# Kernel optimization log

Hardware: AMD Instinct MI355X
Metric: run time of the kernel (lower is better)

The kernel has to match this reference:

```python
import jax, jax.numpy as jnp
import numpy as np

M, N, D, H, R = 16384, 32, 128, 8, 237
Dh = D // H
SCALE = Dh ** -0.5
LN_EPS = 1e-5


def setup_inputs() -> dict:
    key = jax.random.key(0)
    ks = jax.random.split(key, 12)
    entity_repr = jax.random.normal(ks[0], (M, D), dtype=jnp.float32)
    neighbor_index = jax.random.randint(ks[1], (M, N), 0, M, dtype=jnp.int64)
    rel_ids = jax.random.randint(ks[2], (M, N), 0, R, dtype=jnp.int64)
    neighbor_mask = jax.random.randint(ks[3], (M, N), 0, 2, dtype=jnp.int32).astype(bool)
    neighbor_mask = neighbor_mask.at[:, 0].set(True)  # ensure >=1 valid neighbor per node
    s = 1.0 / np.sqrt(D)
    # weights stored in right-multiply form: y = x @ W + b
    Wq = jax.random.normal(ks[4], (D, D), dtype=jnp.float32) * s
    Wk = jax.random.normal(ks[5], (D, D), dtype=jnp.float32) * s
    Wv = jax.random.normal(ks[6], (D, D), dtype=jnp.float32) * s
    Wo = jax.random.normal(ks[7], (D, D), dtype=jnp.float32) * s
    bq = jnp.zeros((D,), jnp.float32)
    bk = jnp.zeros((D,), jnp.float32)
    bv = jnp.zeros((D,), jnp.float32)
    bo = jnp.zeros((D,), jnp.float32)
    rel_table = jax.random.normal(ks[8], (R, D), dtype=jnp.float32)
    ln_gamma = jnp.ones((D,), jnp.float32)
    ln_beta = jnp.zeros((D,), jnp.float32)
    return {
        "entity_repr": entity_repr, "neighbor_index": neighbor_index,
        "rel_ids": rel_ids, "neighbor_mask": neighbor_mask,
        "Wq": Wq, "bq": bq, "Wk": Wk, "bk": bk, "Wv": Wv, "bv": bv,
        "Wo": Wo, "bo": bo, "rel_table": rel_table,
        "ln_gamma": ln_gamma, "ln_beta": ln_beta,
    }


def _layernorm(x, gamma, beta):
    mu = jnp.mean(x, axis=-1, keepdims=True)
    var = jnp.var(x, axis=-1, keepdims=True)
    return (x - mu) * jax.lax.rsqrt(var + LN_EPS) * gamma + beta


def reference(entity_repr, neighbor_index, rel_ids, neighbor_mask,
              Wq, bq, Wk, bk, Wv, bv, Wo, bo, rel_table, ln_gamma, ln_beta):
    valid = neighbor_mask
    safe_index = jnp.where(valid, neighbor_index, 0)
    safe_rel = jnp.where(valid, rel_ids, 0)
    neighbor_repr = entity_repr[safe_index]          # [M, N, D] irregular gather
    rel_emb = rel_table[safe_rel]                     # [M, N, D]
    q = (entity_repr @ Wq + bq).reshape(M, H, Dh)     # [M, H, Dh] (query len 1)
    k = ((neighbor_repr + rel_emb) @ Wk + bk).reshape(M, N, H, Dh)
    v = (neighbor_repr @ Wv + bv).reshape(M, N, H, Dh)
    attn = jnp.einsum("mhd,mnhd->mhn", q, k) * SCALE  # [M, H, N]
    attn = jnp.where(valid[:, None, :], attn, -jnp.inf)
    attn = jax.nn.softmax(attn, axis=-1)
    attn = jnp.nan_to_num(attn, nan=0.0)
    out = jnp.einsum("mhn,mnhd->mhd", attn, v).reshape(M, D)
    out = out @ Wo + bo
    return _layernorm(entity_repr + out, ln_gamma, ln_beta)
```

## Files before the change

kernel.cpp:

```cpp
#include <hip/hip_runtime.h>

#define M_NODES 16384
#define NNBR 32
#define RREL 237
#define ATTN_SCALE 0.25f
#define LN_EPS 1e-5f

typedef float float4v __attribute__((ext_vector_type(4)));
typedef float float2v __attribute__((ext_vector_type(2)));
typedef unsigned int uint4v __attribute__((ext_vector_type(4)));
typedef short short8 __attribute__((ext_vector_type(8)));
typedef float floatx4 __attribute__((ext_vector_type(4)));

__device__ __forceinline__ float bfu2f(unsigned short u) {
    return __builtin_bit_cast(float, ((unsigned int)u) << 16);
}
__device__ __forceinline__ unsigned short f2bfu(float f) {
    unsigned int x = __builtin_bit_cast(unsigned int, f);
    unsigned int lsb = (x >> 16) & 1u;
    x += 0x7fffu + lsb;
    return (unsigned short)(x >> 16);
}
__device__ __forceinline__ unsigned int pack2(float a, float b) {
    return (unsigned int)f2bfu(a) | ((unsigned int)f2bfu(b) << 16);
}
__device__ __forceinline__ float unpk_lo(unsigned int u) {
    return __builtin_bit_cast(float, u << 16);
}
__device__ __forceinline__ float unpk_hi(unsigned int u) {
    return __builtin_bit_cast(float, u & 0xffff0000u);
}


__global__ __launch_bounds__(256) void transpose_w4(
    const float* __restrict__ Wq, const float* __restrict__ Wk,
    const float* __restrict__ Wv, const float* __restrict__ Wo,
    unsigned short* __restrict__ WqT, unsigned short* __restrict__ WkT,
    unsigned short* __restrict__ WvT, unsigned short* __restrict__ WoT) {
    int mat  = blockIdx.x >> 3;
    int slab = blockIdx.x & 7;
    const float* W = (mat == 0) ? Wq : (mat == 1) ? Wk : (mat == 2) ? Wv : Wo;
    unsigned short* WT = (mat == 0) ? WqT : (mat == 1) ? WkT : (mat == 2) ? WvT : WoT;
    int t = threadIdx.x;
    #pragma unroll
    for (int i = 0; i < 8; ++i) {
        int idx = t + 256 * i;
        int r = slab * 16 + (idx >> 7);
        int c = idx & 127;
        WT[c * 128 + r] = f2bfu(W[r * 128 + c]);
    }
}

__device__ __forceinline__ void mfma_core(
    const float* __restrict__ A, const unsigned short* __restrict__ WT,
    int arows, int rbase, unsigned short* lw, floatx4 acc[2][8]) {
    int t = threadIdx.x;
    #pragma unroll
    for (int i = 0; i < 8; ++i) {
        int ci = t + 256 * i;
        int r  = ci >> 4;
        int c8 = ci & 15;
        *(short8*)&lw[r * 136 + c8 * 8] = *(const short8*)&WT[r * 128 + c8 * 8];
    }
    __syncthreads();

    int wave = t >> 6, lane = t & 63;
    int lm = lane & 15, quad = lane >> 4;
    int m0 = rbase + wave * 32;

    #pragma unroll
    for (int i = 0; i < 2; ++i)
        #pragma unroll
        for (int c = 0; c < 8; ++c) acc[i][c] = (floatx4){0.f, 0.f, 0.f, 0.f};

    int r0 = m0 + lm;      if (r0 >= arows) r0 = arows - 1;
    int r1 = m0 + 16 + lm; if (r1 >= arows) r1 = arows - 1;

    #pragma unroll
    for (int ks = 0; ks < 4; ++ks) {
        int koff = ks * 32 + quad * 8;
        float4v f00 = *(const float4v*)&A[r0 * 128 + koff];
        float4v f01 = *(const float4v*)&A[r0 * 128 + koff + 4];
        float4v f10 = *(const float4v*)&A[r1 * 128 + koff];
        float4v f11 = *(const float4v*)&A[r1 * 128 + koff + 4];
        short8 a0, a1;
        #pragma unroll
        for (int j = 0; j < 4; ++j) {
            a0[j]     = (short)f2bfu(f00[j]);
            a0[4 + j] = (short)f2bfu(f01[j]);
            a1[j]     = (short)f2bfu(f10[j]);
            a1[4 + j] = (short)f2bfu(f11[j]);
        }
        #pragma unroll
        for (int c = 0; c < 8; ++c) {
            short8 b = *(const short8*)&lw[(c * 16 + lm) * 136 + koff];
            acc[0][c] = __builtin_amdgcn_mfma_f32_16x16x32_bf16(a0, b, acc[0][c], 0, 0, 0);
            acc[1][c] = __builtin_amdgcn_mfma_f32_16x16x32_bf16(a1, b, acc[1][c], 0, 0, 0);
        }
    }
}

__global__ __launch_bounds__(256) void gemm4_mfma(
    const float* __restrict__ entity, const float* __restrict__ rel_table,
    const unsigned short* __restrict__ WqT, const unsigned short* __restrict__ WkT,
    const unsigned short* __restrict__ WvT,
    const float* __restrict__ bq, const float* __restrict__ bk,
    const float* __restrict__ bv,
    float* __restrict__ EQ, unsigned short* __restrict__ EKV,
    unsigned short* __restrict__ RKb) {
    __shared__ __align__(16) unsigned short lw[128 * 136];

    int y = blockIdx.y;
    const float* A; const unsigned short* WT; const float* bias; int arows;
    unsigned short* outb; int ostride, ooff; int f32out;
    if (y == 0)      { A = entity;    WT = WqT; bias = bq;      arows = M_NODES; outb = nullptr; ostride = 128; ooff = 0;   f32out = 1; }
    else if (y == 1) { A = entity;    WT = WkT; bias = nullptr; arows = M_NODES; outb = EKV;     ostride = 256; ooff = 0;   f32out = 0; }
    else if (y == 2) { A = entity;    WT = WvT; bias = bv;      arows = M_NODES; outb = EKV;     ostride = 256; ooff = 128; f32out = 0; }
    else             { A = rel_table; WT = WkT; bias = bk;      arows = RREL;    outb = RKb;     ostride = 128; ooff = 0;   f32out = 0; }

    int rbase = blockIdx.x * 128;
    if (rbase >= arows) return;

    floatx4 acc[2][8];
    mfma_core(A, WT, arows, rbase, lw, acc);

    int t = threadIdx.x, wave = t >> 6, lane = t & 63;
    int lm = lane & 15, quad = lane >> 4;
    int m0 = rbase + wave * 32;

    #pragma unroll
    for (int c = 0; c < 8; ++c) {
        int col = c * 16 + lm;
        float bb = bias ? bias[col] : 0.0f;
        #pragma unroll
        for (int i = 0; i < 2; ++i) {
            int rb = m0 + i * 16 + quad * 4;
            #pragma unroll
            for (int j = 0; j < 4; ++j) {
                int r = rb + j;
                if (r < arows) {
                    float v = acc[i][c][j] + bb;
                    if (f32out) EQ[r * 128 + col] = v;
                    else        outb[r * ostride + ooff + col] = f2bfu(v);
                }
            }
        }
    }
}

__global__ __launch_bounds__(256) void attn_gather(
    const int* __restrict__ nidx, const int* __restrict__ nrel,
    const int* __restrict__ nmask,
    const float* __restrict__ EQ, const unsigned short* __restrict__ EKV,
    const unsigned short* __restrict__ RKb,
    float* __restrict__ OAT) {
    __shared__ float Pl[4][8][32];
    __shared__ int mix[4][32];

    int w = threadIdx.x >> 6, l = threadIdx.x & 63;
    int m = blockIdx.x * 4 + w;
    int half = l >> 5, n = l & 31;

    int mk = nmask[m * NNBR + n];
    int ix = nidx[m * NNBR + n];
    int ir = nrel[m * NNBR + n];
    if (!mk) { ix = 0; ir = 0; }
    ix = ix < 0 ? 0 : (ix > M_NODES - 1 ? M_NODES - 1 : ix);
    ir = ir < 0 ? 0 : (ir > RREL - 1 ? RREL - 1 : ir);
    if (l < 32) mix[w][l] = ix;

    const float4v* eq4 = (const float4v*)&EQ[m * 128 + half * 64];
    const unsigned short* kp = &EKV[ix * 256 + half * 64];
    const unsigned short* rp = &RKb[ir * 128 + half * 64];
    float acc[4] = {0.f, 0.f, 0.f, 0.f};
    #pragma unroll
    for (int c2 = 0; c2 < 8; ++c2) {
        float4v q0 = eq4[2 * c2], q1 = eq4[2 * c2 + 1];
        short8 k8 = *(const short8*)&kp[c2 * 8];
        short8 r8 = *(const short8*)&rp[c2 * 8];
        int hh = c2 >> 1;
        #pragma unroll
        for (int j = 0; j < 4; ++j) {
            acc[hh] += q0[j] * (bfu2f((unsigned short)k8[j]) + bfu2f((unsigned short)r8[j]));
            acc[hh] += q1[j] * (bfu2f((unsigned short)k8[4 + j]) + bfu2f((unsigned short)r8[4 + j]));
        }
    }
    #pragma unroll
    for (int hh = 0; hh < 4; ++hh) {
        float lf = acc[hh] * ATTN_SCALE;
        if (!mk) lf = -1e30f;
        float mx = lf;
        #pragma unroll
        for (int off = 16; off >= 1; off >>= 1) mx = fmaxf(mx, __shfl_xor(mx, off, 32));
        float p = __expf(lf - mx);
        float s = p;
        #pragma unroll
        for (int off = 16; off >= 1; off >>= 1) s += __shfl_xor(s, off, 32);
        Pl[w][half * 4 + hh][n] = p / s;
    }
    int h0 = l >> 3;
    float o0 = 0.f, o1 = 0.f;
    #pragma unroll 8
    for (int n2 = 0; n2 < 32; ++n2) {
        float pp = Pl[w][h0][n2];
        int ixx = mix[w][n2];
        unsigned int u = *(const unsigned int*)&EKV[ixx * 256 + 128 + 2 * l];
        o0 += pp * unpk_lo(u);
        o1 += pp * unpk_hi(u);
    }
    float2v o; o[0] = o0; o[1] = o1;
    *(float2v*)&OAT[m * 128 + 2 * l] = o;
}

__global__ __launch_bounds__(128) void gemm_wo_ln(
    const float* __restrict__ OAT, const unsigned short* __restrict__ WoT,
    const float* __restrict__ bo, const float* __restrict__ entity,
    const float* __restrict__ gamma_, const float* __restrict__ beta_,
    float* __restrict__ OUT) {
    __shared__ __align__(16) unsigned short lw[128 * 136];

    int t = threadIdx.x;
    #pragma unroll
    for (int i = 0; i < 16; ++i) {
        int ci = t + 128 * i;
        int r  = ci >> 4;
        int c8 = ci & 15;
        *(short8*)&lw[r * 136 + c8 * 8] = *(const short8*)&WoT[r * 128 + c8 * 8];
    }
    __syncthreads();

    int wave = t >> 6, lane = t & 63;
    int lm = lane & 15, quad = lane >> 4;
    int rbase = blockIdx.x * 64;
    int m0 = rbase + wave * 32;

    floatx4 acc[2][8];
    #pragma unroll
    for (int i = 0; i < 2; ++i)
        #pragma unroll
        for (int c = 0; c < 8; ++c) acc[i][c] = (floatx4){0.f, 0.f, 0.f, 0.f};

    int r0 = m0 + lm, r1 = m0 + 16 + lm;
    #pragma unroll
    for (int ks = 0; ks < 4; ++ks) {
        int koff = ks * 32 + quad * 8;
        float4v f00 = *(const float4v*)&OAT[r0 * 128 + koff];
        float4v f01 = *(const float4v*)&OAT[r0 * 128 + koff + 4];
        float4v f10 = *(const float4v*)&OAT[r1 * 128 + koff];
        float4v f11 = *(const float4v*)&OAT[r1 * 128 + koff + 4];
        short8 a0, a1;
        #pragma unroll
        for (int j = 0; j < 4; ++j) {
            a0[j]     = (short)f2bfu(f00[j]);
            a0[4 + j] = (short)f2bfu(f01[j]);
            a1[j]     = (short)f2bfu(f10[j]);
            a1[4 + j] = (short)f2bfu(f11[j]);
        }
        #pragma unroll
        for (int c = 0; c < 8; ++c) {
            short8 b = *(const short8*)&lw[(c * 16 + lm) * 136 + koff];
            acc[0][c] = __builtin_amdgcn_mfma_f32_16x16x32_bf16(a0, b, acc[0][c], 0, 0, 0);
            acc[1][c] = __builtin_amdgcn_mfma_f32_16x16x32_bf16(a1, b, acc[1][c], 0, 0, 0);
        }
    }

    float bb[8], gg[8], be[8];
    #pragma unroll
    for (int c = 0; c < 8; ++c) {
        int col = c * 16 + lm;
        bb[c] = bo[col]; gg[c] = gamma_[col]; be[c] = beta_[col];
    }
    #pragma unroll
    for (int i = 0; i < 2; ++i) {
        #pragma unroll
        for (int j = 0; j < 4; ++j) {
            int r = m0 + i * 16 + quad * 4 + j;
            float y[8];
            float s1 = 0.f, s2 = 0.f;
            #pragma unroll
            for (int c = 0; c < 8; ++c) {
                float v = acc[i][c][j] + bb[c] + entity[r * 128 + c * 16 + lm];
                y[c] = v; s1 += v; s2 += v * v;
            }
            #pragma unroll
            for (int off = 8; off >= 1; off >>= 1) {
                s1 += __shfl_xor(s1, off, 16);
                s2 += __shfl_xor(s2, off, 16);
            }
            float mu  = s1 * (1.0f / 128.0f);
            float var = fmaxf(s2 * (1.0f / 128.0f) - mu * mu, 0.0f);
            float rs  = rsqrtf(var + LN_EPS);
            #pragma unroll
            for (int c = 0; c < 8; ++c)
                OUT[r * 128 + c * 16 + lm] = (y[c] - mu) * rs * gg[c] + be[c];
        }
    }
}

__global__ __launch_bounds__(256, 6) void rga_fused(
    const float* __restrict__ entity,
    const int* __restrict__ nidx,
    const int* __restrict__ nrel,
    const int* __restrict__ nmask,
    const float* __restrict__ Wq, const float* __restrict__ bq,
    const float* __restrict__ Wk, const float* __restrict__ bk,
    const float* __restrict__ Wv, const float* __restrict__ bv,
    const float* __restrict__ Wo, const float* __restrict__ bo,
    const float* __restrict__ rel_table,
    const float* __restrict__ gamma_, const float* __restrict__ beta_,
    float* __restrict__ outp) {
    __shared__ __align__(16) float er[128];
    __shared__ __align__(16) float qv[128];
    __shared__ float qb[8];
    __shared__ __align__(16) float qk[8 * 132];
    __shared__ __align__(16) unsigned int nbvp[32 * 68];
    __shared__ float Lg[8][33];
    __shared__ __align__(16) float pv[8 * 132];
    __shared__ __align__(16) float oat[128];
    __shared__ float ypart[2][128];
    __shared__ float red[4];
    __shared__ int midx[32], mrel[32], mmask[32];

    int m = blockIdx.x;
    int t = threadIdx.x;

    if (t < 32) {
        int mk = nmask[m * NNBR + t];
        int ix = nidx[m * NNBR + t];
        int ir = nrel[m * NNBR + t];
        if (!mk) { ix = 0; ir = 0; }
        ix = ix < 0 ? 0 : (ix > M_NODES - 1 ? M_NODES - 1 : ix);
        ir = ir < 0 ? 0 : (ir > RREL - 1 ? RREL - 1 : ir);
        mmask[t] = mk; midx[t] = ix; mrel[t] = ir;
    }
    if (t >= 128) er[t - 128] = entity[m * 128 + (t - 128)];
    __syncthreads();

    {
        int half = t >> 7, d = t & 127, j0 = half * 64;
        const float4v* e4 = (const float4v*)&er[j0];
        float acc = 0.f;
        #pragma unroll 4
        for (int c = 0; c < 16; ++c) {
            float4v ev = e4[c];
            #pragma unroll
            for (int k = 0; k < 4; ++k)
                acc += ev[k] * Wq[(j0 + c * 4 + k) * 128 + d];
        }
        ypart[half][d] = acc;
    }
    __syncthreads();
    if (t < 128) qv[t] = ypart[0][t] + ypart[1][t] + bq[t];
    __syncthreads();

    #pragma unroll
    for (int rep = 0; rep < 4; ++rep) {
        int o = rep * 256 + t;
        int h = o >> 7, j = o & 127;
        const float4v* wr = (const float4v*)&Wk[j * 128 + h * 16];
        const float4v* q4 = (const float4v*)&qv[h * 16];
        float s = 0.f;
        #pragma unroll
        for (int c = 0; c < 4; ++c) {
            float4v w = wr[c], q = q4[c];
            #pragma unroll
            for (int k = 0; k < 4; ++k) s += w[k] * q[k];
        }
        qk[h * 132 + j] = s;
    }
    if (t < 8) {
        float s = 0.f;
        #pragma unroll
        for (int dh = 0; dh < 16; ++dh) s += qv[t * 16 + dh] * bk[t * 16 + dh];
        qb[t] = s;
    }
    __syncthreads();

    {
        int n = t >> 3, c16 = t & 7, j0 = c16 * 16;
        int ix = midx[n], ir = mrel[n];
        const float4v* ep = (const float4v*)&entity[ix * 128 + j0];
        const float4v* rp = (const float4v*)&rel_table[ir * 128 + j0];
        float ev[16], kv[16];
        #pragma unroll
        for (int c = 0; c < 4; ++c) {
            float4v e4 = ep[c], r4 = rp[c];
            #pragma unroll
            for (int k = 0; k < 4; ++k) {
                ev[c * 4 + k] = e4[k];
                kv[c * 4 + k] = e4[k] + r4[k];
            }
        }
        uint4v u0, u1;
        #pragma unroll
        for (int k = 0; k < 4; ++k) u0[k] = pack2(ev[2 * k], ev[2 * k + 1]);
        #pragma unroll
        for (int k = 0; k < 4; ++k) u1[k] = pack2(ev[8 + 2 * k], ev[9 + 2 * k]);
        *(uint4v*)&nbvp[n * 68 + c16 * 8]     = u0;
        *(uint4v*)&nbvp[n * 68 + c16 * 8 + 4] = u1;
        float acc[8];
        #pragma unroll
        for (int h = 0; h < 8; ++h) {
            const float4v* qrow = (const float4v*)&qk[h * 132 + j0];
            float s = 0.f;
            #pragma unroll
            for (int c = 0; c < 4; ++c) {
                float4v q = qrow[c];
                #pragma unroll
                for (int k = 0; k < 4; ++k) s += q[k] * kv[c * 4 + k];
            }
            acc[h] = s;
        }
        #pragma unroll
        for (int off = 1; off < 8; off <<= 1) {
            #pragma unroll
            for (int h = 0; h < 8; ++h) acc[h] += __shfl_xor(acc[h], off, 8);
        }
        if (c16 == 0) {
            #pragma unroll
            for (int h = 0; h < 8; ++h) {
                float lf = (acc[h] + qb[h]) * ATTN_SCALE;
                if (!mmask[n]) lf = -1e30f;
                Lg[h][n] = lf;
            }
        }
    }
    __syncthreads();

    {
        int h = t >> 5, n = t & 31;
        float lf = Lg[h][n];
        float mx = lf;
        #pragma unroll
        for (int off = 16; off >= 1; off >>= 1) mx = fmaxf(mx, __shfl_xor(mx, off, 32));
        float p = __expf(lf - mx);
        float s = p;
        #pragma unroll
        for (int off = 16; off >= 1; off >>= 1) s += __shfl_xor(s, off, 32);
        Lg[h][n] = p / s;
    }
    __syncthreads();

    {
        int h = t >> 5, c4 = t & 31;
        float4v a = (float4v){0.f, 0.f, 0.f, 0.f};
        #pragma unroll 8
        for (int n = 0; n < 32; ++n) {
            float p = Lg[h][n];
            unsigned int w0 = nbvp[n * 68 + c4 * 2];
            unsigned int w1 = nbvp[n * 68 + c4 * 2 + 1];
            a[0] += p * unpk_lo(w0);
            a[1] += p * unpk_hi(w0);
            a[2] += p * unpk_lo(w1);
            a[3] += p * unpk_hi(w1);
        }
        *(float4v*)&pv[h * 132 + c4 * 4] = a;
    }
    __syncthreads();

    {
        int half = t >> 7, d = t & 127, j0 = half * 64;
        int h = d >> 4;
        const float4v* p4 = (const float4v*)&pv[h * 132 + j0];
        float acc = 0.f;
        #pragma unroll 4
        for (int c = 0; c < 16; ++c) {
            float4v p = p4[c];
            #pragma unroll
            for (int k = 0; k < 4; ++k)
                acc += p[k] * Wv[(j0 + c * 4 + k) * 128 + d];
        }
        ypart[half][d] = acc;
    }
    __syncthreads();
    if (t < 128) oat[t] = ypart[0][t] + ypart[1][t] + bv[t];
    __syncthreads();

    {
        int half = t >> 7, d = t & 127, j0 = half * 64;
        const float4v* o4 = (const float4v*)&oat[j0];
        float acc = 0.f;
        #pragma unroll 4
        for (int c = 0; c < 16; ++c) {
            float4v o = o4[c];
            #pragma unroll
            for (int k = 0; k < 4; ++k)
                acc += o[k] * Wo[(j0 + c * 4 + k) * 128 + d];
        }
        ypart[half][d] = acc;
    }
    __syncthreads();

    float x = 0.f;
    if (t < 128) {
        x = er[t] + ypart[0][t] + ypart[1][t] + bo[t];
        float s1 = x, s2 = x * x;
        #pragma unroll
        for (int off = 32; off >= 1; off >>= 1) {
            s1 += __shfl_xor(s1, off, 64);
            s2 += __shfl_xor(s2, off, 64);
        }
        if ((t & 63) == 0) { red[(t >> 6) * 2] = s1; red[(t >> 6) * 2 + 1] = s2; }
    }
    __syncthreads();
    if (t < 128) {
        float mu  = (red[0] + red[2]) * (1.0f / 128.0f);
        float ms  = (red[1] + red[3]) * (1.0f / 128.0f);
        float var = fmaxf(ms - mu * mu, 0.0f);
        float rs  = rsqrtf(var + LN_EPS);
        outp[m * 128 + t] = (x - mu) * rs * gamma_[t] + beta_[t];
    }
}

extern "C" void kernel_launch(void* const* d_in, const int* in_sizes, int n_in,
                              void* d_out, int out_size, void* d_ws, size_t ws_size,
                              hipStream_t stream) {
    const float* entity    = (const float*)d_in[0];
    const int*   nidx      = (const int*)d_in[1];
    const int*   nrel      = (const int*)d_in[2];
    const int*   nmask     = (const int*)d_in[3];
    const float* Wq        = (const float*)d_in[4];
    const float* bq        = (const float*)d_in[5];
    const float* Wk        = (const float*)d_in[6];
    const float* bk        = (const float*)d_in[7];
    const float* Wv        = (const float*)d_in[8];
    const float* bv        = (const float*)d_in[9];
    const float* Wo        = (const float*)d_in[10];
    const float* bo        = (const float*)d_in[11];
    const float* rel_table = (const float*)d_in[12];
    const float* gamma_    = (const float*)d_in[13];
    const float* beta_     = (const float*)d_in[14];

    char* ws = (char*)d_ws;
    unsigned short* EKV = (unsigned short*)(ws + 0);
    float*          OAT = (float*)(ws + 8388608);
    float*          EQ  = (float*)(ws + 16777216);
    unsigned short* RKb = (unsigned short*)(ws + 25165824);
    unsigned short* WqT = (unsigned short*)(ws + 25226496);
    unsigned short* WkT = (unsigned short*)(ws + 25259264);
    unsigned short* WvT = (unsigned short*)(ws + 25292032);
    unsigned short* WoT = (unsigned short*)(ws + 25324800);
    const size_t NEED = 25357568;

    if (ws_size >= NEED) {
        transpose_w4<<<dim3(32), 256, 0, stream>>>(Wq, Wk, Wv, Wo, WqT, WkT, WvT, WoT);
        gemm4_mfma<<<dim3(128, 4), 256, 0, stream>>>(
            entity, rel_table, WqT, WkT, WvT, bq, bk, bv, EQ, EKV, RKb);
        attn_gather<<<dim3(M_NODES / 4), 256, 0, stream>>>(
            nidx, nrel, nmask, EQ, EKV, RKb, OAT);
        gemm_wo_ln<<<dim3(256), 128, 0, stream>>>(
            OAT, WoT, bo, entity, gamma_, beta_, (float*)d_out);
    } else {
        rga_fused<<<dim3(M_NODES), 256, 0, stream>>>(
            entity, nidx, nrel, nmask, Wq, bq, Wk, bk, Wv, bv, Wo, bo,
            rel_table, gamma_, beta_, (float*)d_out);
    }
}
```

Baseline: 160.5 us.

## Fuse weight transpose into projection GEMM and attention with Wo+LayerNorm

Removes the separate weight-transpose kernel by having each projection block load fp32 weights and convert/transpose them into LDS directly. Fuses the attention-gather kernel with the output projection and LayerNorm: each wave keeps its node's attention output in LDS and runs a single-row MFMA against a per-block bf16 copy of Wo. This drops the OAT intermediate round trip and two launches, but every block now re-converts the weights (including 2048 blocks re-loading Wo), and the Wo MFMA uses only one of 16 rows per tile, wasting matrix throughput.

```diff
diff --git a/kernel.cpp b/kernel.cpp
--- a/kernel.cpp
+++ b/kernel.cpp
@@ -32,35 +32,35 @@
 }
 
 
-__global__ __launch_bounds__(256) void transpose_w4(
-    const float* __restrict__ Wq, const float* __restrict__ Wk,
-    const float* __restrict__ Wv, const float* __restrict__ Wo,
-    unsigned short* __restrict__ WqT, unsigned short* __restrict__ WkT,
-    unsigned short* __restrict__ WvT, unsigned short* __restrict__ WoT) {
-    int mat  = blockIdx.x >> 3;
-    int slab = blockIdx.x & 7;
-    const float* W = (mat == 0) ? Wq : (mat == 1) ? Wk : (mat == 2) ? Wv : Wo;
-    unsigned short* WT = (mat == 0) ? WqT : (mat == 1) ? WkT : (mat == 2) ? WvT : WoT;
+__global__ __launch_bounds__(256) void proj_mfma(
+    const float* __restrict__ entity, const float* __restrict__ rel_table,
+    const float* __restrict__ Wq, const float* __restrict__ bq,
+    const float* __restrict__ Wk, const float* __restrict__ bk,
+    const float* __restrict__ Wv, const float* __restrict__ bv,
+    float* __restrict__ EQ, unsigned short* __restrict__ EKV,
+    unsigned short* __restrict__ RKb) {
+    __shared__ __align__(16) unsigned short lw[128 * 136];
+
+    int y = blockIdx.y;
+    const float* A; const float* Wf; const float* bias; int arows;
+    unsigned short* outb; int ostride, ooff, f32out;
+    if (y == 0)      { A = entity;    Wf = Wq; bias = bq;      arows = M_NODES; outb = nullptr; ostride = 128; ooff = 0;   f32out = 1; }
+    else if (y == 1) { A = entity;    Wf = Wk; bias = nullptr; arows = M_NODES; outb = EKV;     ostride = 256; ooff = 0;   f32out = 0; }
+    else if (y == 2) { A = entity;    Wf = Wv; bias = bv;      arows = M_NODES; outb = EKV;     ostride = 256; ooff = 128; f32out = 0; }
+    else             { A = rel_table; Wf = Wk; bias = bk;      arows = RREL;    outb = RKb;     ostride = 128; ooff = 0;   f32out = 0; }
+
+    int rbase = blockIdx.x * 128;
+    if (rbase >= arows) return;
     int t = threadIdx.x;
-    #pragma unroll
-    for (int i = 0; i < 8; ++i) {
-        int idx = t + 256 * i;
-        int r = slab * 16 + (idx >> 7);
-        int c = idx & 127;
-        WT[c * 128 + r] = f2bfu(W[r * 128 + c]);
-    }
-}
-
-__device__ __forceinline__ void mfma_core(
-    const float* __restrict__ A, const unsigned short* __restrict__ WT,
-    int arows, int rbase, unsigned short* lw, floatx4 acc[2][8]) {
-    int t = threadIdx.x;
-    #pragma unroll
-    for (int i = 0; i < 8; ++i) {
-        int ci = t + 256 * i;
-        int r  = ci >> 4;
-        int c8 = ci & 15;
-        *(short8*)&lw[r * 136 + c8 * 8] = *(const short8*)&WT[r * 128 + c8 * 8];
+
+    #pragma unroll
+    for (int i = 0; i < 16; ++i) {
+        int s = t + i * 256;
+        int k = s >> 5, c4 = s & 31;
+        float4v w = *(const float4v*)&Wf[k * 128 + c4 * 4];
+        #pragma unroll
+        for (int jj = 0; jj < 4; ++jj)
+            lw[(c4 * 4 + jj) * 136 + k] = f2bfu(w[jj]);
     }
     __syncthreads();
 
@@ -68,6 +68,7 @@
     int lm = lane & 15, quad = lane >> 4;
     int m0 = rbase + wave * 32;
 
+    floatx4 acc[2][8];
     #pragma unroll
     for (int i = 0; i < 2; ++i)
         #pragma unroll
@@ -98,35 +99,6 @@
             acc[1][c] = __builtin_amdgcn_mfma_f32_16x16x32_bf16(a1, b, acc[1][c], 0, 0, 0);
         }
     }
-}
-
-__global__ __launch_bounds__(256) void gemm4_mfma(
-    const float* __restrict__ entity, const float* __restrict__ rel_table,
-    const unsigned short* __restrict__ WqT, const unsigned short* __restrict__ WkT,
-    const unsigned short* __restrict__ WvT,
-    const float* __restrict__ bq, const float* __restrict__ bk,
-    const float* __restrict__ bv,
-    float* __restrict__ EQ, unsigned short* __restrict__ EKV,
-    unsigned short* __restrict__ RKb) {
-    __shared__ __align__(16) unsigned short lw[128 * 136];
-
-    int y = blockIdx.y;
-    const float* A; const unsigned short* WT; const float* bias; int arows;
-    unsigned short* outb; int ostride, ooff; int f32out;
-    if (y == 0)      { A = entity;    WT = WqT; bias = bq;      arows = M_NODES; outb = nullptr; ostride = 128; ooff = 0;   f32out = 1; }
-    else if (y == 1) { A = entity;    WT = WkT; bias = nullptr; arows = M_NODES; outb = EKV;     ostride = 256; ooff = 0;   f32out = 0; }
-    else if (y == 2) { A = entity;    WT = WvT; bias = bv;      arows = M_NODES; outb = EKV;     ostride = 256; ooff = 128; f32out = 0; }
-    else             { A = rel_table; WT = WkT; bias = bk;      arows = RREL;    outb = RKb;     ostride = 128; ooff = 0;   f32out = 0; }
-
-    int rbase = blockIdx.x * 128;
-    if (rbase >= arows) return;
-
-    floatx4 acc[2][8];
-    mfma_core(A, WT, arows, rbase, lw, acc);
-
-    int t = threadIdx.x, wave = t >> 6, lane = t & 63;
-    int lm = lane & 15, quad = lane >> 4;
-    int m0 = rbase + wave * 32;
 
     #pragma unroll
     for (int c = 0; c < 8; ++c) {
@@ -148,17 +120,35 @@
     }
 }
 
-__global__ __launch_bounds__(256) void attn_gather(
+__global__ __launch_bounds__(512, 6) void attn_wo_ln(
     const int* __restrict__ nidx, const int* __restrict__ nrel,
     const int* __restrict__ nmask,
     const float* __restrict__ EQ, const unsigned short* __restrict__ EKV,
     const unsigned short* __restrict__ RKb,
-    float* __restrict__ OAT) {
-    __shared__ float Pl[4][8][32];
-    __shared__ int mix[4][32];
-
-    int w = threadIdx.x >> 6, l = threadIdx.x & 63;
-    int m = blockIdx.x * 4 + w;
+    const float* __restrict__ Wo, const float* __restrict__ bo,
+    const float* __restrict__ entity,
+    const float* __restrict__ gamma_, const float* __restrict__ beta_,
+    float* __restrict__ OUT) {
+    __shared__ __align__(16) unsigned short lwWo[128 * 136];
+    __shared__ __align__(16) float oatw[8][132];
+    __shared__ float Pl[8][8][32];
+    __shared__ int mix[8][32];
+
+    int t = threadIdx.x;
+
+    #pragma unroll
+    for (int i = 0; i < 8; ++i) {
+        int s = t + i * 512;
+        int k = s >> 5, c4 = s & 31;
+        float4v w = *(const float4v*)&Wo[k * 128 + c4 * 4];
+        #pragma unroll
+        for (int jj = 0; jj < 4; ++jj)
+            lwWo[(c4 * 4 + jj) * 136 + k] = f2bfu(w[jj]);
+    }
+    __syncthreads();
+
+    int w = t >> 6, l = t & 63;
+    int m = blockIdx.x * 8 + w;
     int half = l >> 5, n = l & 31;
 
     int mk = nmask[m * NNBR + n];
@@ -172,7 +162,7 @@
     const float4v* eq4 = (const float4v*)&EQ[m * 128 + half * 64];
     const unsigned short* kp = &EKV[ix * 256 + half * 64];
     const unsigned short* rp = &RKb[ir * 128 + half * 64];
-    float acc[4] = {0.f, 0.f, 0.f, 0.f};
+    float acl[4] = {0.f, 0.f, 0.f, 0.f};
     #pragma unroll
     for (int c2 = 0; c2 < 8; ++c2) {
         float4v q0 = eq4[2 * c2], q1 = eq4[2 * c2 + 1];
@@ -181,13 +171,13 @@
         int hh = c2 >> 1;
         #pragma unroll
         for (int j = 0; j < 4; ++j) {
-            acc[hh] += q0[j] * (bfu2f((unsigned short)k8[j]) + bfu2f((unsigned short)r8[j]));
-            acc[hh] += q1[j] * (bfu2f((unsigned short)k8[4 + j]) + bfu2f((unsigned short)r8[4 + j]));
+            acl[hh] += q0[j] * (bfu2f((unsigned short)k8[j]) + bfu2f((unsigned short)r8[j]));
+            acl[hh] += q1[j] * (bfu2f((unsigned short)k8[4 + j]) + bfu2f((unsigned short)r8[4 + j]));
         }
     }
     #pragma unroll
     for (int hh = 0; hh < 4; ++hh) {
-        float lf = acc[hh] * ATTN_SCALE;
+        float lf = acl[hh] * ATTN_SCALE;
         if (!mk) lf = -1e30f;
         float mx = lf;
         #pragma unroll
@@ -198,6 +188,7 @@
         for (int off = 16; off >= 1; off >>= 1) s += __shfl_xor(s, off, 32);
         Pl[w][half * 4 + hh][n] = p / s;
     }
+
     int h0 = l >> 3;
     float o0 = 0.f, o1 = 0.f;
     #pragma unroll 8
@@ -208,91 +199,52 @@
         o0 += pp * unpk_lo(u);
         o1 += pp * unpk_hi(u);
     }
-    float2v o; o[0] = o0; o[1] = o1;
-    *(float2v*)&OAT[m * 128 + 2 * l] = o;
-}
-
-__global__ __launch_bounds__(128) void gemm_wo_ln(
-    const float* __restrict__ OAT, const unsigned short* __restrict__ WoT,
-    const float* __restrict__ bo, const float* __restrict__ entity,
-    const float* __restrict__ gamma_, const float* __restrict__ beta_,
-    float* __restrict__ OUT) {
-    __shared__ __align__(16) unsigned short lw[128 * 136];
-
-    int t = threadIdx.x;
-    #pragma unroll
-    for (int i = 0; i < 16; ++i) {
-        int ci = t + 128 * i;
-        int r  = ci >> 4;
-        int c8 = ci & 15;
-        *(short8*)&lw[r * 136 + c8 * 8] = *(const short8*)&WoT[r * 128 + c8 * 8];
-    }
-    __syncthreads();
-
-    int wave = t >> 6, lane = t & 63;
-    int lm = lane & 15, quad = lane >> 4;
-    int rbase = blockIdx.x * 64;
-    int m0 = rbase + wave * 32;
-
-    floatx4 acc[2][8];
-    #pragma unroll
-    for (int i = 0; i < 2; ++i)
-        #pragma unroll
-        for (int c = 0; c < 8; ++c) acc[i][c] = (floatx4){0.f, 0.f, 0.f, 0.f};
-
-    int r0 = m0 + lm, r1 = m0 + 16 + lm;
+    oatw[w][2 * l]     = o0;
+    oatw[w][2 * l + 1] = o1;
+
+    int lm = l & 15, quad = l >> 4;
+    floatx4 acc[8];
+    #pragma unroll
+    for (int c = 0; c < 8; ++c) acc[c] = (floatx4){0.f, 0.f, 0.f, 0.f};
     #pragma unroll
     for (int ks = 0; ks < 4; ++ks) {
         int koff = ks * 32 + quad * 8;
-        float4v f00 = *(const float4v*)&OAT[r0 * 128 + koff];
-        float4v f01 = *(const float4v*)&OAT[r0 * 128 + koff + 4];
-        float4v f10 = *(const float4v*)&OAT[r1 * 128 + koff];
-        float4v f11 = *(const float4v*)&OAT[r1 * 128 + koff + 4];
-        short8 a0, a1;
+        float4v f0 = *(const float4v*)&oatw[w][koff];
+        float4v f1 = *(const float4v*)&oatw[w][koff + 4];
+        short8 a;
         #pragma unroll
         for (int j = 0; j < 4; ++j) {
-            a0[j]     = (short)f2bfu(f00[j]);
-            a0[4 + j] = (short)f2bfu(f01[j]);
-            a1[j]     = (short)f2bfu(f10[j]);
-            a1[4 + j] = (short)f2bfu(f11[j]);
+            a[j]     = (short)f2bfu(f0[j]);
+            a[4 + j] = (short)f2bfu(f1[j]);
         }
         #pragma unroll
         for (int c = 0; c < 8; ++c) {
-            short8 b = *(const short8*)&lw[(c * 16 + lm) * 136 + koff];
-            acc[0][c] = __builtin_amdgcn_mfma_f32_16x16x32_bf16(a0, b, acc[0][c], 0, 0, 0);
-            acc[1][c] = __builtin_amdgcn_mfma_f32_16x16x32_bf16(a1, b, acc[1][c], 0, 0, 0);
-        }
-    }
-
-    float bb[8], gg[8], be[8];
+            short8 b = *(const short8*)&lwWo[(c * 16 + lm) * 136 + koff];
+            acc[c] = __builtin_amdgcn_mfma_f32_16x16x32_bf16(a, b, acc[c], 0, 0, 0);
+        }
+    }
+
+    float yv[8];
+    float s1 = 0.f, s2 = 0.f;
     #pragma unroll
     for (int c = 0; c < 8; ++c) {
         int col = c * 16 + lm;
-        bb[c] = bo[col]; gg[c] = gamma_[col]; be[c] = beta_[col];
-    }
-    #pragma unroll
-    for (int i = 0; i < 2; ++i) {
-        #pragma unroll
-        for (int j = 0; j < 4; ++j) {
-            int r = m0 + i * 16 + quad * 4 + j;
-            float y[8];
-            float s1 = 0.f, s2 = 0.f;
-            #pragma unroll
-            for (int c = 0; c < 8; ++c) {
-                float v = acc[i][c][j] + bb[c] + entity[r * 128 + c * 16 + lm];
-                y[c] = v; s1 += v; s2 += v * v;
-            }
-            #pragma unroll
-            for (int off = 8; off >= 1; off >>= 1) {
-                s1 += __shfl_xor(s1, off, 16);
-                s2 += __shfl_xor(s2, off, 16);
-            }
-            float mu  = s1 * (1.0f / 128.0f);
-            float var = fmaxf(s2 * (1.0f / 128.0f) - mu * mu, 0.0f);
-            float rs  = rsqrtf(var + LN_EPS);
-            #pragma unroll
-            for (int c = 0; c < 8; ++c)
-                OUT[r * 128 + c * 16 + lm] = (y[c] - mu) * rs * gg[c] + be[c];
+        float v = acc[c][0] + bo[col] + entity[m * 128 + col];
+        yv[c] = v; s1 += v; s2 += v * v;
+    }
+    #pragma unroll
+    for (int off = 8; off >= 1; off >>= 1) {
+        s1 += __shfl_xor(s1, off, 16);
+        s2 += __shfl_xor(s2, off, 16);
+    }
+    float mu  = s1 * (1.0f / 128.0f);
+    float var = fmaxf(s2 * (1.0f / 128.0f) - mu * mu, 0.0f);
+    float rs  = rsqrtf(var + LN_EPS);
+    if (quad == 0) {
+        #pragma unroll
+        for (int c = 0; c < 8; ++c) {
+            int col = c * 16 + lm;
+            OUT[m * 128 + col] = (yv[c] - mu) * rs * gamma_[col] + beta_[col];
         }
     }
 }
@@ -362,9 +314,9 @@
         float s = 0.f;
         #pragma unroll
         for (int c = 0; c < 4; ++c) {
-            float4v w = wr[c], q = q4[c];
-            #pragma unroll
-            for (int k = 0; k < 4; ++k) s += w[k] * q[k];
+            float4v ww = wr[c], q = q4[c];
+            #pragma unroll
+            for (int k = 0; k < 4; ++k) s += ww[k] * q[k];
         }
         qk[h * 132 + j] = s;
     }
@@ -533,23 +485,16 @@
 
     char* ws = (char*)d_ws;
     unsigned short* EKV = (unsigned short*)(ws + 0);
-    float*          OAT = (float*)(ws + 8388608);
-    float*          EQ  = (float*)(ws + 16777216);
-    unsigned short* RKb = (unsigned short*)(ws + 25165824);
-    unsigned short* WqT = (unsigned short*)(ws + 25226496);
-    unsigned short* WkT = (unsigned short*)(ws + 25259264);
-    unsigned short* WvT = (unsigned short*)(ws + 25292032);
-    unsigned short* WoT = (unsigned short*)(ws + 25324800);
-    const size_t NEED = 25357568;
+    float*          EQ  = (float*)(ws + 8388608);
+    unsigned short* RKb = (unsigned short*)(ws + 16777216);
+    const size_t NEED = 16777216 + 60672;
 
     if (ws_size >= NEED) {
-        transpose_w4<<<dim3(32), 256, 0, stream>>>(Wq, Wk, Wv, Wo, WqT, WkT, WvT, WoT);
-        gemm4_mfma<<<dim3(128, 4), 256, 0, stream>>>(
-            entity, rel_table, WqT, WkT, WvT, bq, bk, bv, EQ, EKV, RKb);
-        attn_gather<<<dim3(M_NODES / 4), 256, 0, stream>>>(
-            nidx, nrel, nmask, EQ, EKV, RKb, OAT);
-        gemm_wo_ln<<<dim3(256), 128, 0, stream>>>(
-            OAT, WoT, bo, entity, gamma_, beta_, (float*)d_out);
+        proj_mfma<<<dim3(128, 4), 256, 0, stream>>>(
+            entity, rel_table, Wq, bq, Wk, bk, Wv, bv, EQ, EKV, RKb);
+        attn_wo_ln<<<dim3(M_NODES / 8), 512, 0, stream>>>(
+            nidx, nrel, nmask, EQ, EKV, RKb, Wo, bo, entity, gamma_, beta_,
+            (float*)d_out);
     } else {
         rga_fused<<<dim3(M_NODES), 256, 0, stream>>>(
             entity, nidx, nrel, nmask, Wq, bq, Wk, bk, Wv, bv, Wo, bo,
```

After: 179.5 us. +11.8%, slower.

## Store Q and attention output as bf16 and widen value gather loads

Applied to the files above, without the earlier changes.

The Q projection and the attention output are now stored in bf16 instead of fp32. This halves the intermediate traffic between the projection GEMM, the attention gather and the Wo GEMM, and removes the fp32-to-bf16 conversion in the final GEMM. The value aggregation is reorganised so each lane loads 8 bf16 values (16 bytes) per neighbour over a subset of neighbours, then reduces across lane groups with shuffles. The softmax scratch array is padded to avoid LDS bank conflicts. Q is rounded to bf16 before the score dot product, which adds a small accuracy loss.

```diff
diff --git a/kernel.cpp b/kernel.cpp
--- a/kernel.cpp
+++ b/kernel.cpp
@@ -7,7 +7,7 @@
 #define LN_EPS 1e-5f
 
 typedef float float4v __attribute__((ext_vector_type(4)));
-typedef float float2v __attribute__((ext_vector_type(2)));
+typedef unsigned int uint2v __attribute__((ext_vector_type(2)));
 typedef unsigned int uint4v __attribute__((ext_vector_type(4)));
 typedef short short8 __attribute__((ext_vector_type(8)));
 typedef float floatx4 __attribute__((ext_vector_type(4)));
@@ -32,7 +32,7 @@
 }
 
 
-__global__ __launch_bounds__(256) void transpose_w4(
+__global__ __launch_bounds__(256) void prep_w(
     const float* __restrict__ Wq, const float* __restrict__ Wk,
     const float* __restrict__ Wv, const float* __restrict__ Wo,
     unsigned short* __restrict__ WqT, unsigned short* __restrict__ WkT,
@@ -51,10 +51,28 @@
     }
 }
 
-__device__ __forceinline__ void mfma_core(
-    const float* __restrict__ A, const unsigned short* __restrict__ WT,
-    int arows, int rbase, unsigned short* lw, floatx4 acc[2][8]) {
+__global__ __launch_bounds__(256) void gemm4_mfma(
+    const float* __restrict__ entity, const float* __restrict__ rel_table,
+    const unsigned short* __restrict__ WqT, const unsigned short* __restrict__ WkT,
+    const unsigned short* __restrict__ WvT,
+    const float* __restrict__ bq, const float* __restrict__ bk,
+    const float* __restrict__ bv,
+    unsigned short* __restrict__ EQb, unsigned short* __restrict__ EKV,
+    unsigned short* __restrict__ RKb) {
+    __shared__ __align__(16) unsigned short lw[128 * 136];
+
+    int y = blockIdx.y;
+    const float* A; const unsigned short* WT; const float* bias; int arows;
+    unsigned short* outb; int ostride, ooff;
+    if (y == 0)      { A = entity;    WT = WqT; bias = bq;      arows = M_NODES; outb = EQb; ostride = 128; ooff = 0;   }
+    else if (y == 1) { A = entity;    WT = WkT; bias = nullptr; arows = M_NODES; outb = EKV; ostride = 256; ooff = 0;   }
+    else if (y == 2) { A = entity;    WT = WvT; bias = bv;      arows = M_NODES; outb = EKV; ostride = 256; ooff = 128; }
+    else             { A = rel_table; WT = WkT; bias = bk;      arows = RREL;    outb = RKb; ostride = 128; ooff = 0;   }
+
+    int rbase = blockIdx.x * 128;
+    if (rbase >= arows) return;
     int t = threadIdx.x;
+
     #pragma unroll
     for (int i = 0; i < 8; ++i) {
         int ci = t + 256 * i;
@@ -68,6 +86,7 @@
     int lm = lane & 15, quad = lane >> 4;
     int m0 = rbase + wave * 32;
 
+    floatx4 acc[2][8];
     #pragma unroll
     for (int i = 0; i < 2; ++i)
         #pragma unroll
@@ -98,35 +117,6 @@
             acc[1][c] = __builtin_amdgcn_mfma_f32_16x16x32_bf16(a1, b, acc[1][c], 0, 0, 0);
         }
     }
-}
-
-__global__ __launch_bounds__(256) void gemm4_mfma(
-    const float* __restrict__ entity, const float* __restrict__ rel_table,
-    const unsigned short* __restrict__ WqT, const unsigned short* __restrict__ WkT,
-    const unsigned short* __restrict__ WvT,
-    const float* __restrict__ bq, const float* __restrict__ bk,
-    const float* __restrict__ bv,
-    float* __restrict__ EQ, unsigned short* __restrict__ EKV,
-    unsigned short* __restrict__ RKb) {
-    __shared__ __align__(16) unsigned short lw[128 * 136];
-
-    int y = blockIdx.y;
-    const float* A; const unsigned short* WT; const float* bias; int arows;
-    unsigned short* outb; int ostride, ooff; int f32out;
-    if (y == 0)      { A = entity;    WT = WqT; bias = bq;      arows = M_NODES; outb = nullptr; ostride = 128; ooff = 0;   f32out = 1; }
-    else if (y == 1) { A = entity;    WT = WkT; bias = nullptr; arows = M_NODES; outb = EKV;     ostride = 256; ooff = 0;   f32out = 0; }
-    else if (y == 2) { A = entity;    WT = WvT; bias = bv;      arows = M_NODES; outb = EKV;     ostride = 256; ooff = 128; f32out = 0; }
-    else             { A = rel_table; WT = WkT; bias = bk;      arows = RREL;    outb = RKb;     ostride = 128; ooff = 0;   f32out = 0; }
-
-    int rbase = blockIdx.x * 128;
-    if (rbase >= arows) return;
-
-    floatx4 acc[2][8];
-    mfma_core(A, WT, arows, rbase, lw, acc);
-
-    int t = threadIdx.x, wave = t >> 6, lane = t & 63;
-    int lm = lane & 15, quad = lane >> 4;
-    int m0 = rbase + wave * 32;
 
     #pragma unroll
     for (int c = 0; c < 8; ++c) {
@@ -138,11 +128,7 @@
             #pragma unroll
             for (int j = 0; j < 4; ++j) {
                 int r = rb + j;
-                if (r < arows) {
-                    float v = acc[i][c][j] + bb;
-                    if (f32out) EQ[r * 128 + col] = v;
-                    else        outb[r * ostride + ooff + col] = f2bfu(v);
-                }
+                if (r < arows) outb[r * ostride + ooff + col] = f2bfu(acc[i][c][j] + bb);
             }
         }
     }
@@ -151,10 +137,10 @@
 __global__ __launch_bounds__(256) void attn_gather(
     const int* __restrict__ nidx, const int* __restrict__ nrel,
     const int* __restrict__ nmask,
-    const float* __restrict__ EQ, const unsigned short* __restrict__ EKV,
+    const unsigned short* __restrict__ EQb, const unsigned short* __restrict__ EKV,
     const unsigned short* __restrict__ RKb,
-    float* __restrict__ OAT) {
-    __shared__ float Pl[4][8][32];
+    unsigned short* __restrict__ OATb) {
+    __shared__ float Pl[4][8][33];
     __shared__ int mix[4][32];
 
     int w = threadIdx.x >> 6, l = threadIdx.x & 63;
@@ -169,21 +155,20 @@
     ir = ir < 0 ? 0 : (ir > RREL - 1 ? RREL - 1 : ir);
     if (l < 32) mix[w][l] = ix;
 
-    const float4v* eq4 = (const float4v*)&EQ[m * 128 + half * 64];
+    const unsigned short* qp = &EQb[m * 128 + half * 64];
     const unsigned short* kp = &EKV[ix * 256 + half * 64];
     const unsigned short* rp = &RKb[ir * 128 + half * 64];
     float acc[4] = {0.f, 0.f, 0.f, 0.f};
     #pragma unroll
-    for (int c2 = 0; c2 < 8; ++c2) {
-        float4v q0 = eq4[2 * c2], q1 = eq4[2 * c2 + 1];
-        short8 k8 = *(const short8*)&kp[c2 * 8];
-        short8 r8 = *(const short8*)&rp[c2 * 8];
-        int hh = c2 >> 1;
-        #pragma unroll
-        for (int j = 0; j < 4; ++j) {
-            acc[hh] += q0[j] * (bfu2f((unsigned short)k8[j]) + bfu2f((unsigned short)r8[j]));
-            acc[hh] += q1[j] * (bfu2f((unsigned short)k8[4 + j]) + bfu2f((unsigned short)r8[4 + j]));
-        }
+    for (int c = 0; c < 8; ++c) {
+        short8 q8 = *(const short8*)&qp[c * 8];
+        short8 k8 = *(const short8*)&kp[c * 8];
+        short8 r8 = *(const short8*)&rp[c * 8];
+        int hh = c >> 1;
+        #pragma unroll
+        for (int j = 0; j < 8; ++j)
+            acc[hh] += bfu2f((unsigned short)q8[j]) *
+                       (bfu2f((unsigned short)k8[j]) + bfu2f((unsigned short)r8[j]));
     }
     #pragma unroll
     for (int hh = 0; hh < 4; ++hh) {
@@ -198,22 +183,34 @@
         for (int off = 16; off >= 1; off >>= 1) s += __shfl_xor(s, off, 32);
         Pl[w][half * 4 + hh][n] = p / s;
     }
-    int h0 = l >> 3;
-    float o0 = 0.f, o1 = 0.f;
-    #pragma unroll 8
-    for (int n2 = 0; n2 < 32; ++n2) {
-        float pp = Pl[w][h0][n2];
+
+    int dgrp = l & 15, ngrp = l >> 4;
+    int h = dgrp >> 1;
+    float o[8] = {0.f, 0.f, 0.f, 0.f, 0.f, 0.f, 0.f, 0.f};
+    #pragma unroll
+    for (int i = 0; i < 8; ++i) {
+        int n2 = ngrp + i * 4;
+        float pp = Pl[w][h][n2];
         int ixx = mix[w][n2];
-        unsigned int u = *(const unsigned int*)&EKV[ixx * 256 + 128 + 2 * l];
-        o0 += pp * unpk_lo(u);
-        o1 += pp * unpk_hi(u);
-    }
-    float2v o; o[0] = o0; o[1] = o1;
-    *(float2v*)&OAT[m * 128 + 2 * l] = o;
+        short8 v8 = *(const short8*)&EKV[ixx * 256 + 128 + dgrp * 8];
+        #pragma unroll
+        for (int j = 0; j < 8; ++j) o[j] += pp * bfu2f((unsigned short)v8[j]);
+    }
+    #pragma unroll
+    for (int j = 0; j < 8; ++j) {
+        o[j] += __shfl_xor(o[j], 16, 64);
+        o[j] += __shfl_xor(o[j], 32, 64);
+    }
+    if (ngrp == 0) {
+        uint4v u;
+        u[0] = pack2(o[0], o[1]); u[1] = pack2(o[2], o[3]);
+        u[2] = pack2(o[4], o[5]); u[3] = pack2(o[6], o[7]);
+        *(uint4v*)&OATb[m * 128 + dgrp * 8] = u;
+    }
 }
 
 __global__ __launch_bounds__(128) void gemm_wo_ln(
-    const float* __restrict__ OAT, const unsigned short* __restrict__ WoT,
+    const unsigned short* __restrict__ OATb, const unsigned short* __restrict__ WoT,
     const float* __restrict__ bo, const float* __restrict__ entity,
     const float* __restrict__ gamma_, const float* __restrict__ beta_,
     float* __restrict__ OUT) {
@@ -244,18 +241,8 @@
     #pragma unroll
     for (int ks = 0; ks < 4; ++ks) {
         int koff = ks * 32 + quad * 8;
-        float4v f00 = *(const float4v*)&OAT[r0 * 128 + koff];
-        float4v f01 = *(const float4v*)&OAT[r0 * 128 + koff + 4];
-        float4v f10 = *(const float4v*)&OAT[r1 * 128 + koff];
-        float4v f11 = *(const float4v*)&OAT[r1 * 128 + koff + 4];
-        short8 a0, a1;
-        #pragma unroll
-        for (int j = 0; j < 4; ++j) {
-            a0[j]     = (short)f2bfu(f00[j]);
-            a0[4 + j] = (short)f2bfu(f01[j]);
-            a1[j]     = (short)f2bfu(f10[j]);
-            a1[4 + j] = (short)f2bfu(f11[j]);
-        }
+        short8 a0 = *(const short8*)&OATb[r0 * 128 + koff];
+        short8 a1 = *(const short8*)&OATb[r1 * 128 + koff];
         #pragma unroll
         for (int c = 0; c < 8; ++c) {
             short8 b = *(const short8*)&lw[(c * 16 + lm) * 136 + koff];
@@ -297,6 +284,7 @@
     }
 }
 
+typedef unsigned int uint4f __attribute__((ext_vector_type(4)));
 __global__ __launch_bounds__(256, 6) void rga_fused(
     const float* __restrict__ entity,
     const int* __restrict__ nidx,
@@ -362,9 +350,9 @@
         float s = 0.f;
         #pragma unroll
         for (int c = 0; c < 4; ++c) {
-            float4v w = wr[c], q = q4[c];
-            #pragma unroll
-            for (int k = 0; k < 4; ++k) s += w[k] * q[k];
+            float4v ww = wr[c], q = q4[c];
+            #pragma unroll
+            for (int k = 0; k < 4; ++k) s += ww[k] * q[k];
         }
         qk[h * 132 + j] = s;
     }
@@ -391,13 +379,13 @@
                 kv[c * 4 + k] = e4[k] + r4[k];
             }
         }
-        uint4v u0, u1;
+        uint4f u0, u1;
         #pragma unroll
         for (int k = 0; k < 4; ++k) u0[k] = pack2(ev[2 * k], ev[2 * k + 1]);
         #pragma unroll
         for (int k = 0; k < 4; ++k) u1[k] = pack2(ev[8 + 2 * k], ev[9 + 2 * k]);
-        *(uint4v*)&nbvp[n * 68 + c16 * 8]     = u0;
-        *(uint4v*)&nbvp[n * 68 + c16 * 8 + 4] = u1;
+        *(uint4f*)&nbvp[n * 68 + c16 * 8]     = u0;
+        *(uint4f*)&nbvp[n * 68 + c16 * 8 + 4] = u1;
         float acc[8];
         #pragma unroll
         for (int h = 0; h < 8; ++h) {
@@ -532,24 +520,24 @@
     const float* beta_     = (const float*)d_in[14];
 
     char* ws = (char*)d_ws;
-    unsigned short* EKV = (unsigned short*)(ws + 0);
-    float*          OAT = (float*)(ws + 8388608);
-    float*          EQ  = (float*)(ws + 16777216);
-    unsigned short* RKb = (unsigned short*)(ws + 25165824);
-    unsigned short* WqT = (unsigned short*)(ws + 25226496);
-    unsigned short* WkT = (unsigned short*)(ws + 25259264);
-    unsigned short* WvT = (unsigned short*)(ws + 25292032);
-    unsigned short* WoT = (unsigned short*)(ws + 25324800);
-    const size_t NEED = 25357568;
+    unsigned short* EKV  = (unsigned short*)(ws + 0);
+    unsigned short* EQb  = (unsigned short*)(ws + 8388608);
+    unsigned short* OATb = (unsigned short*)(ws + 12582912);
+    unsigned short* RKb  = (unsigned short*)(ws + 16777216);
+    unsigned short* WqT  = (unsigned short*)(ws + 16837888);
+    unsigned short* WkT  = (unsigned short*)(ws + 16870656);
+    unsigned short* WvT  = (unsigned short*)(ws + 16903424);
+    unsigned short* WoT  = (unsigned short*)(ws + 16936192);
+    const size_t NEED = 16968960;
 
     if (ws_size >= NEED) {
-        transpose_w4<<<dim3(32), 256, 0, stream>>>(Wq, Wk, Wv, Wo, WqT, WkT, WvT, WoT);
+        prep_w<<<dim3(32), 256, 0, stream>>>(Wq, Wk, Wv, Wo, WqT, WkT, WvT, WoT);
         gemm4_mfma<<<dim3(128, 4), 256, 0, stream>>>(
-            entity, rel_table, WqT, WkT, WvT, bq, bk, bv, EQ, EKV, RKb);
+            entity, rel_table, WqT, WkT, WvT, bq, bk, bv, EQb, EKV, RKb);
         attn_gather<<<dim3(M_NODES / 4), 256, 0, stream>>>(
-            nidx, nrel, nmask, EQ, EKV, RKb, OAT);
+            nidx, nrel, nmask, EQb, EKV, RKb, OATb);
         gemm_wo_ln<<<dim3(256), 128, 0, stream>>>(
-            OAT, WoT, bo, entity, gamma_, beta_, (float*)d_out);
+            OATb, WoT, bo, entity, gamma_, beta_, (float*)d_out);
     } else {
         rga_fused<<<dim3(M_NODES), 256, 0, stream>>>(
             entity, nidx, nrel, nmask, Wq, bq, Wk, bk, Wv, bv, Wo, bo,
```

New measurement: 154.1 us. 4.0% less time.
